# Performance work log

Hardware: AMD Instinct MI355X
Metric: run time of the kernel (lower is better)

## Reference

```python
import jax, jax.numpy as jnp
import numpy as np
from jax import lax

EPS = 1e-08


def setup_inputs() -> dict:
    key = jax.random.key(0)
    k1, k2, k3 = jax.random.split(key, 3)
    B, Cin, Cout, K, H, W = 8, 512, 512, 3, 64, 64
    feature_map = jax.random.normal(k1, (B, Cin, H, W), dtype=jnp.float32)
    style = jax.random.normal(k2, (B, Cin), dtype=jnp.float32)
    weight = jax.random.normal(k3, (Cout, Cin, K, K), dtype=jnp.float32)
    return {"feature_map": feature_map, "style": style, "weight": weight}


def reference(feature_map, style, weight):
    # EqualizedWeight: scale raw N(0,1) weight by 1/sqrt(fan_in)
    Cout, Cin, K, _ = weight.shape
    gain = 1.0 / np.sqrt(Cin * K * K)
    w = weight * gain  # (O, I, K, K)

    # Modulate: per-sample scale of input channels -> (B, O, I, K, K)
    w = w[None] * style[:, None, :, None, None]

    # Demodulate: normalize each (b, o) filter to unit norm
    sigma_inv = lax.rsqrt(jnp.sum(w * w, axis=(2, 3, 4), keepdims=True) + EPS)
    w = w * sigma_inv

    # Per-sample conv2d, padding 'same' (equivalent to the groups=B trick)
    def conv_one(x, wi):  # x: (I, H, W), wi: (O, I, K, K)
        return lax.conv_general_dilated(
            x[None], wi, window_strides=(1, 1), padding="SAME",
            dimension_numbers=("NCHW", "OIHW", "NCHW"))[0]

    return jax.vmap(conv_one)(feature_map, w)  # (B, O, H, W)
```

## Files before the change

kernel.cpp:

```cpp
#include <hip/hip_runtime.h>

typedef unsigned short u16;
typedef __attribute__((ext_vector_type(8))) short s16x8;
typedef __attribute__((ext_vector_type(4))) float floatx4;

#define XT_ROWELEMS 2112
#define XT_CGELEMS  139392
#define XT_PB       4460544ull
#define WM_ELEMS    2359296ull
#define WM_PB       4718592ull

#define GLDS(gp, lp) __builtin_amdgcn_global_load_lds(                      \
    (const __attribute__((address_space(1))) void*)(gp),                    \
    (__attribute__((address_space(3))) void*)(lp), 16, 0, 0)

__device__ __forceinline__ u16 f2bf(float f) {
  union { float f; unsigned u; } x; x.f = f;
  unsigned r = x.u + 0x7fffu + ((x.u >> 16) & 1u);
  return (u16)(r >> 16);
}

__global__ __launch_bounds__(256) void prep_fused(
    const float* __restrict__ fm, const float* __restrict__ w,
    const float* __restrict__ style, u16* __restrict__ xt,
    u16* __restrict__ wm, int b0)
{
  __shared__ __align__(16) char smraw[18448];
  const int bid = blockIdx.x;
  const int g = bid / 3, rrole = bid - g * 3;
  const int tid = threadIdx.x;

  if (rrole < 2) {
    float* sm = (float*)smraw;
    const int ti = g * 2 + rrole;
    const int y = ti & 63, cg = (ti >> 6) & 15, bl = ti >> 10;
    const int x = tid & 63, cq = tid >> 6;
    const float* src = fm + (((size_t)(b0 + bl) * 512 + cg * 32) * 64 + y) * 64;
#pragma unroll
    for (int j = 0; j < 8; ++j) {
      int ci = j * 4 + cq;
      sm[x * 33 + ci] = src[(size_t)ci * 4096 + x];
    }

    u16* cgbase = xt + (size_t)(bl * 16 + cg) * XT_CGELEMS;
    const uint4 z = {0u, 0u, 0u, 0u};
    u16* rowb = cgbase + (size_t)(y + 1) * XT_ROWELEMS;
    if (tid < 4)              ((uint4*)rowb)[tid] = z;
    else if (tid < 8)         ((uint4*)(rowb + 65 * 32))[tid - 4] = z;
    if (y == 0)  for (int i = tid; i < 264; i += 256) ((uint4*)cgbase)[i] = z;
    if (y == 63) for (int i = tid; i < 264; i += 256) ((uint4*)(cgbase + 65 * XT_ROWELEMS))[i] = z;

    __syncthreads();
    union { u16 s[8]; uint4 v; } u;
#pragma unroll
    for (int j = 0; j < 8; ++j) {
      int e = tid * 8 + j;
      u.s[j] = f2bf(sm[(e >> 5) * 33 + (e & 31)]);
    }
    const int col = 1 + (tid >> 2);
    const int slot = (tid & 3) ^ ((col >> 1) & 3);
    ((uint4*)rowb)[col * 4 + slot] = u.v;
  } else {
    float* sv = (float*)smraw;
    float* red = (float*)(smraw + 18432);
    const int o = g & 511, bl = g >> 9;
    const float gain = 0.014731391f;
    const float* wo = w + (size_t)o * 4608;
    const float* st = style + (size_t)(b0 + bl) * 512;
    float ss = 0.f;
#pragma unroll
    for (int j = 0; j < 18; ++j) {
      int idx = j * 256 + tid;
      float v = wo[idx] * gain * st[idx / 9];
      sv[idx] = v;
      ss += v * v;
    }
#pragma unroll
    for (int off = 32; off > 0; off >>= 1) ss += __shfl_down(ss, off, 64);
    if ((tid & 63) == 0) red[tid >> 6] = ss;
    __syncthreads();
    float sinv = rsqrtf(red[0] + red[1] + red[2] + red[3] + 1e-8f);
    const int axor = ((o >> 1) & 3) << 3;
    u16* base = wm + (size_t)bl * WM_ELEMS + (size_t)o * 32;
#pragma unroll
    for (int j = 0; j < 18; ++j) {
      int e = j * 256 + tid;
      int t = e >> 9, c = e & 511;
      base[((size_t)(t * 16 + (c >> 5))) * 16384 + ((c & 31) ^ axor)] = f2bf(sv[c * 9 + t] * sinv);
    }
  }
}

__global__ __launch_bounds__(256, 2) void conv_mfma(
    const u16* __restrict__ Wmod, const u16* __restrict__ xt,
    float* __restrict__ out, int b0, int nb)
{
  const int id = blockIdx.x;
  const int bl = id % nb;
  const int rest = id / nb;
  const int og = rest & 1, p_blk = rest >> 1;
  const int tid = threadIdx.x;
  const int lane = tid & 63, wave = tid >> 6;
  const int wm_off = (wave & 1) * 128, wn_off = (wave >> 1) * 64;
  const int l15 = lane & 15, quad = lane >> 4;

  __shared__ __align__(16) u16 As[2][8192];
  __shared__ __align__(16) u16 Bs[8448];

  const int y0 = p_blk * 2;
  const size_t xt_base = ((size_t)(bl * 16) * XT_CGELEMS) + (size_t)y0 * XT_ROWELEMS;
  const size_t w_base = (size_t)bl * WM_ELEMS + (size_t)og * (256 * 32);

  auto stage_b = [&](int cg) {
    const char* g = (const char*)(xt + xt_base + (size_t)cg * XT_CGELEMS);
    for (int r = wave; r < 16; r += 4)
      GLDS(g + r * 1024 + lane * 16, (char*)Bs + r * 1024);
    if (wave == 0 && lane < 32)
      GLDS(g + 16384 + lane * 16, (char*)Bs + 16384);
  };
  auto stage_a = [&](int t, int cg, int buf) {
    const char* g = (const char*)(Wmod + w_base + (size_t)(t * 16 + cg) * 16384);
    for (int r = wave; r < 16; r += 4)
      GLDS(g + r * 1024 + lane * 16, (char*)As[buf] + r * 1024);
  };

  int aoff[8];
#pragma unroll
  for (int mt = 0; mt < 8; ++mt) {
    int row = wm_off + mt * 16 + l15;
    aoff[mt] = row * 32 + ((quad ^ ((row >> 1) & 3)) << 3);
  }
  int pr[4], pc[4];
#pragma unroll
  for (int nt = 0; nt < 4; ++nt) {
    int p = wn_off + nt * 16 + l15;
    pr[nt] = p >> 6; pc[nt] = p & 63;
  }

  floatx4 acc[8][4];
  const floatx4 zf = {0.f, 0.f, 0.f, 0.f};
#pragma unroll
  for (int mt = 0; mt < 8; ++mt)
#pragma unroll
    for (int nt = 0; nt < 4; ++nt) acc[mt][nt] = zf;

  stage_b(0);
  stage_a(0, 0, 0);
  __syncthreads();

#pragma unroll 1
  for (int cg = 0; cg < 16; ++cg) {
#pragma unroll 1
    for (int t = 0; t < 9; ++t) {
      const int cur = (cg * 9 + t) & 1, nxt = cur ^ 1;
      const bool last = (cg == 15 && t == 8);
      const bool cgb = (t == 8 && cg < 15);
      if (!last) stage_a(t < 8 ? t + 1 : 0, t < 8 ? cg : cg + 1, nxt);

      const int ky = t / 3, kx = t - ky * 3;
      s16x8 afr[8], bfr[4];
      const u16* Ab = As[cur];
#pragma unroll
      for (int nt = 0; nt < 4; ++nt) {
        int r = pr[nt] + ky, c = pc[nt] + kx;
        bfr[nt] = *(const s16x8*)&Bs[(r * 66 + c) * 32 + ((quad ^ ((c >> 1) & 3)) << 3)];
      }
#pragma unroll
      for (int mt = 0; mt < 8; ++mt)
        afr[mt] = *(const s16x8*)&Ab[aoff[mt]];
#pragma unroll
      for (int mt = 0; mt < 8; ++mt)
#pragma unroll
        for (int nt = 0; nt < 4; ++nt)
          acc[mt][nt] = __builtin_amdgcn_mfma_f32_16x16x32_bf16(
              afr[mt], bfr[nt], acc[mt][nt], 0, 0, 0);

      if (cgb) {
        __syncthreads();
        stage_b(cg + 1);
      }
      __syncthreads();
    }
  }

  float* outp = out + ((size_t)(b0 + bl) * 512 + og * 256) * 4096 + p_blk * 128;
#pragma unroll
  for (int mt = 0; mt < 8; ++mt)
#pragma unroll
    for (int nt = 0; nt < 4; ++nt) {
      int n = wn_off + nt * 16 + l15;
#pragma unroll
      for (int r = 0; r < 4; ++r) {
        int m = wm_off + mt * 16 + quad * 4 + r;
        outp[(size_t)m * 4096 + n] = acc[mt][nt][r];
      }
    }
}

__global__ __launch_bounds__(256) void conv_direct(
    const float* __restrict__ fm, const float* __restrict__ style,
    const float* __restrict__ w, float* __restrict__ out)
{
  const int o = blockIdx.x, b = blockIdx.y, tid = threadIdx.x;
  __shared__ float swm[4608];
  __shared__ float red[4];
  const float gain = 0.014731391f;
  const float* wo = w + (size_t)o * 4608;
  const float* st = style + (size_t)b * 512;
  float ss = 0.f;
#pragma unroll
  for (int j = 0; j < 18; ++j) {
    int idx = j * 256 + tid;
    float v = wo[idx] * gain * st[idx / 9];
    swm[idx] = v;
    ss += v * v;
  }
#pragma unroll
  for (int off = 32; off > 0; off >>= 1) ss += __shfl_down(ss, off, 64);
  if ((tid & 63) == 0) red[tid >> 6] = ss;
  __syncthreads();
  const float sinv = rsqrtf(red[0] + red[1] + red[2] + red[3] + 1e-8f);

  const int y = tid >> 2, x0 = (tid & 3) * 16;
  float acc[16];
#pragma unroll
  for (int i = 0; i < 16; ++i) acc[i] = 0.f;
  const float* fb = fm + (size_t)b * 512 * 4096;
  for (int ci = 0; ci < 512; ++ci) {
    const float* fc = fb + (size_t)ci * 4096;
    const float* wr = swm + ci * 9;
#pragma unroll
    for (int ky = 0; ky < 3; ++ky) {
      int yy = y + ky - 1;
      if (yy < 0 || yy > 63) continue;
      const float* frow = fc + yy * 64;
#pragma unroll
      for (int kx = 0; kx < 3; ++kx) {
        float wv = wr[ky * 3 + kx];
#pragma unroll
        for (int i = 0; i < 16; ++i) {
          int xx = x0 + i + kx - 1;
          float xv = (xx >= 0 && xx < 64) ? frow[xx] : 0.f;
          acc[i] += wv * xv;
        }
      }
    }
  }
  float* op = out + ((size_t)b * 512 + o) * 4096 + y * 64 + x0;
#pragma unroll
  for (int i = 0; i < 16; ++i) op[i] = acc[i] * sinv;
}

extern "C" void kernel_launch(void* const* d_in, const int* in_sizes, int n_in,
                              void* d_out, int out_size, void* d_ws, size_t ws_size,
                              hipStream_t stream) {
  const float* fm = (const float*)d_in[0];
  const float* style = (const float*)d_in[1];
  const float* w = (const float*)d_in[2];
  float* out = (float*)d_out;

  if (ws_size < XT_PB + WM_PB) {
    conv_direct<<<dim3(512, 8), 256, 0, stream>>>(fm, style, w, out);
    return;
  }
  int nb = 8;
  while (nb > 1 && (size_t)nb * (XT_PB + WM_PB) > ws_size) nb >>= 1;

  u16* xt = (u16*)d_ws;
  u16* wmod = (u16*)((char*)d_ws + (size_t)nb * XT_PB);

  for (int b0 = 0; b0 < 8; b0 += nb) {
    prep_fused<<<dim3(1536 * nb), 256, 0, stream>>>(fm, w, style, xt, wmod, b0);
    conv_mfma<<<dim3(64 * nb), 256, 0, stream>>>(wmod, xt, out, b0, nb);
  }
}
```

Baseline: 268.0 us.

## Restructure conv MFMA into 8-wave blocks with triple-buffered A and phased pipeline

The conv kernel moves to 512-thread blocks that each cover four output rows (256 pixels), halving the grid. The weight tile becomes triple-buffered and the input tile double-buffered. Loads are split into per-phase chunks interleaved with MFMA pairs, using explicit s_waitcnt vmcnt, s_barrier, sched_barrier and setprio. The goal is to overlap global-to-LDS copies with matrix math and remove full __syncthreads stalls. In exchange it uses more LDS per block and depends on hand-tuned vmcnt counts, which are fragile.

Result: slower. 291.6 us (+8.8%).

```diff
diff --git a/kernel.cpp b/kernel.cpp
--- a/kernel.cpp
+++ b/kernel.cpp
@@ -13,6 +13,8 @@
 #define GLDS(gp, lp) __builtin_amdgcn_global_load_lds(                      \
     (const __attribute__((address_space(1))) void*)(gp),                    \
     (__attribute__((address_space(3))) void*)(lp), 16, 0, 0)
+
+#define WAITVM(N) asm volatile("s_waitcnt vmcnt(" #N ")" ::: "memory")
 
 __device__ __forceinline__ u16 f2bf(float f) {
   union { float f; unsigned u; } x; x.f = f;
@@ -91,7 +93,7 @@
   }
 }
 
-__global__ __launch_bounds__(256, 2) void conv_mfma(
+__global__ __launch_bounds__(512, 2) void conv_mfma(
     const u16* __restrict__ Wmod, const u16* __restrict__ xt,
     float* __restrict__ out, int b0, int nb)
 {
@@ -104,24 +106,24 @@
   const int wm_off = (wave & 1) * 128, wn_off = (wave >> 1) * 64;
   const int l15 = lane & 15, quad = lane >> 4;
 
-  __shared__ __align__(16) u16 As[2][8192];
-  __shared__ __align__(16) u16 Bs[8448];
-
-  const int y0 = p_blk * 2;
+  __shared__ __align__(16) u16 As[3][8192];
+  __shared__ __align__(16) u16 Bs[2][12672];
+
+  const int y0 = p_blk * 4;
   const size_t xt_base = ((size_t)(bl * 16) * XT_CGELEMS) + (size_t)y0 * XT_ROWELEMS;
   const size_t w_base = (size_t)bl * WM_ELEMS + (size_t)og * (256 * 32);
 
-  auto stage_b = [&](int cg) {
+  auto stage_b = [&](int cg, int half, int k) {
     const char* g = (const char*)(xt + xt_base + (size_t)cg * XT_CGELEMS);
-    for (int r = wave; r < 16; r += 4)
-      GLDS(g + r * 1024 + lane * 16, (char*)Bs + r * 1024);
-    if (wave == 0 && lane < 32)
-      GLDS(g + 16384 + lane * 16, (char*)Bs + 16384);
+    char* l = (char*)Bs[half];
+    const int off = wave * 3168 + k * 1024;
+    if (k < 3)            GLDS(g + off + lane * 16, l + off);
+    else if (lane < 6)    GLDS(g + off + lane * 16, l + off);
   };
-  auto stage_a = [&](int t, int cg, int buf) {
+  auto stage_a = [&](int t, int cg, int buf, int k) {
     const char* g = (const char*)(Wmod + w_base + (size_t)(t * 16 + cg) * 16384);
-    for (int r = wave; r < 16; r += 4)
-      GLDS(g + r * 1024 + lane * 16, (char*)As[buf] + r * 1024);
+    const int off = k * 8192 + wave * 1024;
+    GLDS(g + off + lane * 16, (char*)As[buf] + off);
   };
 
   int aoff[8];
@@ -144,46 +146,100 @@
 #pragma unroll
     for (int nt = 0; nt < 4; ++nt) acc[mt][nt] = zf;
 
-  stage_b(0);
-  stage_a(0, 0, 0);
-  __syncthreads();
+#define MFMA_PAIR(M0, A0, A1)                                                  \
+  _Pragma("unroll")                                                            \
+  for (int nt = 0; nt < 4; ++nt) {                                             \
+    acc[M0][nt] = __builtin_amdgcn_mfma_f32_16x16x32_bf16(A0, bfr[nt],         \
+                                                          acc[M0][nt], 0, 0, 0); \
+    acc[M0 + 1][nt] = __builtin_amdgcn_mfma_f32_16x16x32_bf16(A1, bfr[nt],     \
+                                                          acc[M0 + 1][nt], 0, 0, 0); \
+  }
+
+#define PHASE(M0, I0, I1, STAGE_STMT)                                          \
+  {                                                                            \
+    s16x8 a0 = *(const s16x8*)&Acur[aoff[I0]];                                 \
+    s16x8 a1 = *(const s16x8*)&Acur[aoff[I1]];                                 \
+    STAGE_STMT;                                                                \
+    __builtin_amdgcn_s_barrier();                                              \
+    asm volatile("s_waitcnt lgkmcnt(0)");                                      \
+    __builtin_amdgcn_sched_barrier(0);                                         \
+    __builtin_amdgcn_s_setprio(1);                                             \
+    MFMA_PAIR(M0, a0, a1);                                                     \
+    __builtin_amdgcn_s_setprio(0);                                             \
+    __builtin_amdgcn_s_barrier();                                              \
+  }
+#define PHASE_END(M0, I0, I1, VMSTMT)                                          \
+  {                                                                            \
+    s16x8 a0 = *(const s16x8*)&Acur[aoff[I0]];                                 \
+    s16x8 a1 = *(const s16x8*)&Acur[aoff[I1]];                                 \
+    __builtin_amdgcn_s_barrier();                                              \
+    asm volatile("s_waitcnt lgkmcnt(0)");                                      \
+    __builtin_amdgcn_sched_barrier(0);                                         \
+    __builtin_amdgcn_s_setprio(1);                                             \
+    MFMA_PAIR(M0, a0, a1);                                                     \
+    __builtin_amdgcn_s_setprio(0);                                             \
+    VMSTMT;                                                                    \
+    __builtin_amdgcn_s_barrier();                                              \
+  }
+
+  stage_b(0, 0, 0); stage_b(0, 0, 1); stage_b(0, 0, 2); stage_b(0, 0, 3);
+  stage_a(0, 0, 0, 0); stage_a(0, 0, 0, 1);
+  stage_a(1, 0, 1, 0); stage_a(1, 0, 1, 1);
+  WAITVM(2);
+  __builtin_amdgcn_s_barrier();
 
 #pragma unroll 1
-  for (int cg = 0; cg < 16; ++cg) {
-#pragma unroll 1
+  for (int cg = 0; cg < 15; ++cg) {
+    const int cgp = cg & 1, cgn = cgp ^ 1;
+    const u16* Bcur = Bs[cgp];
+#pragma unroll
     for (int t = 0; t < 9; ++t) {
-      const int cur = (cg * 9 + t) & 1, nxt = cur ^ 1;
-      const bool last = (cg == 15 && t == 8);
-      const bool cgb = (t == 8 && cg < 15);
-      if (!last) stage_a(t < 8 ? t + 1 : 0, t < 8 ? cg : cg + 1, nxt);
-
+      const int cur = t % 3, nx2 = (t + 2) % 3;
+      const int t2 = (t + 2 < 9) ? t + 2 : t - 7;
+      const int cg2 = (t + 2 < 9) ? cg : cg + 1;
       const int ky = t / 3, kx = t - ky * 3;
-      s16x8 afr[8], bfr[4];
-      const u16* Ab = As[cur];
+      const u16* Acur = As[cur];
+
+      s16x8 bfr[4];
 #pragma unroll
       for (int nt = 0; nt < 4; ++nt) {
         int r = pr[nt] + ky, c = pc[nt] + kx;
-        bfr[nt] = *(const s16x8*)&Bs[(r * 66 + c) * 32 + ((quad ^ ((c >> 1) & 3)) << 3)];
+        bfr[nt] = *(const s16x8*)&Bcur[(r * 66 + c) * 32 + ((quad ^ ((c >> 1) & 3)) << 3)];
       }
-#pragma unroll
-      for (int mt = 0; mt < 8; ++mt)
-        afr[mt] = *(const s16x8*)&Ab[aoff[mt]];
-#pragma unroll
-      for (int mt = 0; mt < 8; ++mt)
-#pragma unroll
-        for (int nt = 0; nt < 4; ++nt)
-          acc[mt][nt] = __builtin_amdgcn_mfma_f32_16x16x32_bf16(
-              afr[mt], bfr[nt], acc[mt][nt], 0, 0, 0);
-
-      if (cgb) {
-        __syncthreads();
-        stage_b(cg + 1);
+      PHASE(0, 0, 1, stage_a(t2, cg2, nx2, 0));
+      PHASE(2, 2, 3, stage_a(t2, cg2, nx2, 1));
+      PHASE(4, 4, 5, if (t >= 3 && t <= 6) stage_b(cg + 1, cgn, t - 3));
+      if (t == 3)                 { PHASE_END(6, 6, 7, WAITVM(3)); }
+      else if (t >= 4 && t <= 6)  { PHASE_END(6, 6, 7, WAITVM(4)); }
+      else                        { PHASE_END(6, 6, 7, WAITVM(2)); }
+    }
+  }
+  {
+    const u16* Bcur = Bs[15 & 1];
+#pragma unroll
+    for (int t = 0; t < 9; ++t) {
+      const int cur = t % 3, nx2 = (t + 2) % 3;
+      const int ky = t / 3, kx = t - ky * 3;
+      const u16* Acur = As[cur];
+      s16x8 bfr[4];
+#pragma unroll
+      for (int nt = 0; nt < 4; ++nt) {
+        int r = pr[nt] + ky, c = pc[nt] + kx;
+        bfr[nt] = *(const s16x8*)&Bcur[(r * 66 + c) * 32 + ((quad ^ ((c >> 1) & 3)) << 3)];
       }
-      __syncthreads();
-    }
-  }
-
-  float* outp = out + ((size_t)(b0 + bl) * 512 + og * 256) * 4096 + p_blk * 128;
+      PHASE(0, 0, 1, if (t <= 6) stage_a(t + 2, 15, nx2, 0));
+      PHASE(2, 2, 3, if (t <= 6) stage_a(t + 2, 15, nx2, 1));
+      PHASE(4, 4, 5, );
+      if (t <= 6)       { PHASE_END(6, 6, 7, WAITVM(2)); }
+      else if (t == 7)  { PHASE_END(6, 6, 7, WAITVM(0)); }
+      else              { PHASE_END(6, 6, 7, ); }
+    }
+  }
+#undef PHASE
+#undef PHASE_END
+#undef MFMA_PAIR
+
+  float* outp = out + ((size_t)(b0 + bl) * 512 + og * 256) * 4096 + p_blk * 256;
 #pragma unroll
   for (int mt = 0; mt < 8; ++mt)
 #pragma unroll
@@ -271,6 +327,6 @@
 
   for (int b0 = 0; b0 < 8; b0 += nb) {
     prep_fused<<<dim3(1536 * nb), 256, 0, stream>>>(fm, w, style, xt, wmod, b0);
-    conv_mfma<<<dim3(64 * nb), 256, 0, stream>>>(wmod, xt, out, b0, nb);
-  }
-}
+    conv_mfma<<<dim3(32 * nb), 512, 0, stream>>>(wmod, xt, out, b0, nb);
+  }
+}
```
